# Performance work log

Hardware: AMD Instinct MI355X
Metric: run time of the kernel (lower is better)

## Reference

```python
import jax, jax.numpy as jnp
import numpy as np

H, B, S, E, V, C = 1024, 1024, 128, 6, 3, 10


def setup_inputs() -> dict:
    key = jax.random.key(0)
    ks = jax.random.split(key, 18)
    sH = 1.0 / np.sqrt(H)

    def n(k, shape, scale):
        return (jax.random.normal(k, shape, dtype=jnp.float32) * scale)

    return {
        'x': jax.random.randint(ks[0], (B, S), 0, V),
        'emb': n(ks[1], (V, E), 1.0),
        'W_gx': n(ks[2], (H, E), 1.0 / np.sqrt(E)),
        'W_gh': n(ks[3], (H, H), sH),
        'b_g': n(ks[4], (H, 1), sH),
        'W_ix': n(ks[5], (H, E), 1.0 / np.sqrt(E)),
        'W_ih': n(ks[6], (H, H), sH),
        'b_i': n(ks[7], (H, 1), sH),
        'W_fx': n(ks[8], (H, E), 1.0 / np.sqrt(E)),
        'W_fh': n(ks[9], (H, H), sH),
        'b_f': n(ks[10], (H, 1), sH),
        'W_ox': n(ks[11], (H, E), 1.0 / np.sqrt(E)),
        'W_oh': n(ks[12], (H, H), sH),
        'b_o': n(ks[13], (H, 1), sH),
        'W_ph': n(ks[14], (C, H), sH),
        'b_p': n(ks[15], (C, 1), sH),
        'h_init': n(ks[16], (H, B), 1.0),
        'c_init': n(ks[17], (H, B), 1.0),
    }


def reference(x, emb, W_gx, W_gh, b_g, W_ix, W_ih, b_i, W_fx, W_fh, b_f,
              W_ox, W_oh, b_o, W_ph, b_p, h_init, c_init):
    T = x.shape[1] - 1  # torch loop runs over seq_length - 1 steps
    e = emb[x[:, :T]]  # [B, T, E]
    # Precompute all input-to-gate projections in one batched contraction each.
    Xg = jnp.einsum('he,bte->thb', W_gx, e)  # [T, H, B]
    Xi = jnp.einsum('he,bte->thb', W_ix, e)
    Xf = jnp.einsum('he,bte->thb', W_fx, e)
    Xo = jnp.einsum('he,bte->thb', W_ox, e)

    def step(carry, xs):
        h, c = carry  # [H, B]
        xg, xi, xf, xo = xs
        g = jnp.tanh(xg + W_gh @ h + b_g)
        i = jax.nn.sigmoid(xi + W_ih @ h + b_i)
        f = jax.nn.sigmoid(xf + W_fh @ h + b_f)
        o = jax.nn.sigmoid(xo + W_oh @ h + b_o)
        c2 = g * i + c * f
        h2 = jnp.tanh(c2) * o
        return (h2, c2), None

    (h, c), _ = jax.lax.scan(step, (h_init, c_init), (Xg, Xi, Xf, Xo))
    p = W_ph @ h + b_p  # [C, B]
    return jax.nn.log_softmax(p.T, axis=-1)  # [B, C]
```

## Files before the change

### kernel.cpp

```cpp
#include <hip/hip_runtime.h>

constexpr int kH = 1024;
constexpr int kB = 1024;
constexpr int kS = 128;
constexpr int kT = 127;
constexpr int kE = 6;
constexpr int kV = 3;
constexpr int kC = 10;

typedef short s16x8 __attribute__((ext_vector_type(8)));
typedef short s16x4 __attribute__((ext_vector_type(4)));
typedef float f32x4 __attribute__((ext_vector_type(4)));
typedef int   i32x2 __attribute__((ext_vector_type(2)));
typedef int   i32x4 __attribute__((ext_vector_type(4)));
typedef unsigned short u16;

__device__ __forceinline__ float b2f(u16 u) {
    return __uint_as_float(((unsigned)u) << 16);
}
__device__ __forceinline__ u16 f2b(float f) {
    unsigned u = __float_as_uint(f);
    return (u16)((u + 0x7FFFu + ((u >> 16) & 1u)) >> 16);
}
__device__ __forceinline__ float sigmoid_fast(float x) {
    return 1.0f / (1.0f + __expf(-x));
}
__device__ __forceinline__ float tanh_fast(float x) {
    return 2.0f / (1.0f + __expf(-2.0f * x)) - 1.0f;
}
__device__ __forceinline__ float clamp30(float x) {
    return fminf(fmaxf(x, -30.0f), 30.0f);
}

__device__ __forceinline__ void async_copy16(const u16* g, u16* l) {
    __builtin_amdgcn_global_load_lds(
        (const __attribute__((address_space(1))) void*)g,
        (__attribute__((address_space(3))) void*)l, 16, 0, 0);
}

__global__ __launch_bounds__(256) void prep_weights(
    const float* __restrict__ Wgh, const float* __restrict__ Wih,
    const float* __restrict__ Wfh, const float* __restrict__ Woh,
    u16* __restrict__ wsw)
{
    unsigned grp = blockIdx.x * 256 + threadIdx.x;
    const int lane = grp & 63;
    const int lm   = lane & 15;
    const int quad = lane >> 4;
    const int k0   = (grp >> 6) & 7;
    const int g    = (grp >> 9) & 3;
    const int kc   = (grp >> 11) & 3;
    const int by   = grp >> 13;
    const float* src = (g == 0) ? Wgh : (g == 1) ? Wih : (g == 2) ? Wfh : Woh;
    const int row = by * 16 + lm;
    const int k   = kc * 256 + k0 * 32 + quad * 8;
    f32x4 v0 = *(const f32x4*)(src + (size_t)row * kH + k);
    f32x4 v1 = *(const f32x4*)(src + (size_t)row * kH + k + 4);
    s16x8 o;
#pragma unroll
    for (int j = 0; j < 4; ++j) o[j] = (short)f2b(v0[j]);
#pragma unroll
    for (int j = 0; j < 4; ++j) o[4 + j] = (short)f2b(v1[j]);
    *(s16x8*)(wsw + (size_t)grp * 8) = o;
}

__global__ __launch_bounds__(1024) void prep_hc(
    const float* __restrict__ h0, const float* __restrict__ c0,
    u16* __restrict__ hA, float* __restrict__ cT)
{
    __shared__ float th[32][33];
    __shared__ float tc[32][33];
    int b = blockIdx.x * 32 + threadIdx.x;
    int h = blockIdx.y * 32 + threadIdx.y;
    th[threadIdx.y][threadIdx.x] = h0[(size_t)h * kB + b];
    tc[threadIdx.y][threadIdx.x] = c0[(size_t)h * kB + b];
    __syncthreads();
    int ob = blockIdx.x * 32 + threadIdx.y;
    int oh = blockIdx.y * 32 + threadIdx.x;
    hA[(size_t)ob * kH + oh] = f2b(th[threadIdx.x][threadIdx.y]);
    cT[(size_t)ob * kH + oh] = tc[threadIdx.x][threadIdx.y];
}

__global__ __launch_bounds__(256) void prep_q(
    const float* __restrict__ Wgx, const float* __restrict__ Wix,
    const float* __restrict__ Wfx, const float* __restrict__ Wox,
    const float* __restrict__ bg,  const float* __restrict__ bi,
    const float* __restrict__ bf_, const float* __restrict__ bo,
    const float* __restrict__ emb, float* __restrict__ Qp,
    int* __restrict__ ctrl)
{
    int tid = blockIdx.x * blockDim.x + threadIdx.x;
    if (tid < 512) ctrl[tid] = 0;
    if (tid >= 4096) return;
    int g   = tid >> 10;
    int hr4 = (tid & 1023) >> 2;
    int v   = tid & 3;
    const float* Wx = (g == 0) ? Wgx : (g == 1) ? Wix : (g == 2) ? Wfx : Wox;
    const float* bb = (g == 0) ? bg  : (g == 1) ? bi  : (g == 2) ? bf_ : bo;
    f32x4 o;
#pragma unroll
    for (int reg = 0; reg < 4; ++reg) {
        int row = hr4 * 4 + reg;
        float s = bb[row];
        if (v < kV) {
#pragma unroll
            for (int e = 0; e < kE; ++e) s += Wx[row * kE + e] * emb[v * kE + e];
        }
        o[reg] = s;
    }
    *(f32x4*)(Qp + (size_t)tid * 4) = o;
}

__global__ __launch_bounds__(512, 2) void lstm_persist(
    const u16* __restrict__ wsw, const float* __restrict__ Qp,
    const int* __restrict__ x,
    short* __restrict__ hA, short* __restrict__ hB,
    const float* __restrict__ cT, int* __restrict__ ctrl,
    u16* __restrict__ xcb)
{
    __shared__ u16 wlds[65536];
    __shared__ int sh_ids[2];

    const int tid  = threadIdx.x;
    const int lane = tid & 63;
    const int wave = tid >> 6;
    const int lm   = lane & 15;
    const int quad = lane >> 4;

    if (tid == 0) {
        unsigned xccr;
        asm volatile("s_getreg_b32 %0, hwreg(HW_REG_XCC_ID)" : "=s"(xccr));
        int rank = atomicAdd(ctrl + 264 + (xccr & 7), 1);
        sh_ids[0] = (int)(xccr & 7);
        sh_ids[1] = rank;
    }
    __syncthreads();
    const int xcc   = sh_ids[0];
    const int rank  = sh_ids[1];
    const int p     = xcc >> 1;
    const int side  = xcc & 1;
    const int q     = side * 32 + rank;
    const int qprt  = (1 - side) * 32 + rank;
    const int r0 = q * 16;
    const int cl0 = wave * 32;
    const int c0 = p * 256 + cl0;

    int* pflag = ctrl;
    int* lcnt  = ctrl + 256;

    const u16* wswblk = wsw + (size_t)q * 65536;

#pragma unroll
    for (int rr = 0; rr < 16; ++rr) {
        const int ub = wave * 8192 + rr * 512;
        async_copy16(wswblk + ub + lane * 8, &wlds[ub]);
    }

    f32x4 creg[2];
#pragma unroll
    for (int nt = 0; nt < 2; ++nt)
        creg[nt] = *(const f32x4*)(cT +
            (size_t)(c0 + nt * 16 + lm) * kH + r0 + quad * 4);

    const int* xp0 = x + (size_t)(c0 + lm) * kS;
    const int* xp1 = x + (size_t)(c0 + 16 + lm) * kS;
    const int koff = quad * 8;

    asm volatile("s_waitcnt vmcnt(0)" ::: "memory");
    __syncthreads();

#pragma unroll 1
    for (int t = 0; t < kT; ++t) {
        short* hout = (t & 1) ? hA : hB;
        u16* xw = xcb + (size_t)(xcc * 2 + ((t + 1) & 1)) * 262144;

        if (t >= 1) {
            if (tid == 0) {
                const int* cp = lcnt + xcc;
                const int tgt = 64 * t;
                for (;;) {
                    int v;
                    asm volatile("global_load_dword %0, %1, off sc0 sc1\n\t"
                                 "s_waitcnt vmcnt(0)"
                                 : "=v"(v) : "v"(cp) : "memory");
                    if (v >= tgt) break;
                    __builtin_amdgcn_s_sleep(1);
                }
            }
            __syncthreads();
            asm volatile("buffer_inv" ::: "memory");
        }

        const u16* xr = xcb + (size_t)(xcc * 2 + (t & 1)) * 262144;
        const u16* hrow0;
        const u16* hrow1;
        if (t == 0) {
            hrow0 = (const u16*)hA + (size_t)(c0 + lm) * kH + koff;
            hrow1 = (const u16*)hA + (size_t)(c0 + 16 + lm) * kH + koff;
        } else {
            hrow0 = xr + (size_t)(cl0 + lm) * kH + koff;
            hrow1 = xr + (size_t)(cl0 + 16 + lm) * kH + koff;
        }

        s16x8 br[8][2];
#pragma unroll
        for (int s = 0; s < 6; ++s) {
            br[s][0] = *(const s16x8*)(hrow0 + s * 32);
            br[s][1] = *(const s16x8*)(hrow1 + s * 32);
        }

        int vv[2];
        {
            int v0 = xp0[t]; vv[0] = (v0 < 0) ? 0 : (v0 > kV - 1) ? (kV - 1) : v0;
            int v1 = xp1[t]; vv[1] = (v1 < 0) ? 0 : (v1 > kV - 1) ? (kV - 1) : v1;
        }
        f32x4 qv[2][4];
#pragma unroll
        for (int nt = 0; nt < 2; ++nt)
#pragma unroll
            for (int g = 0; g < 4; ++g)
                qv[nt][g] = *(const f32x4*)(Qp +
                    (size_t)(((g * 256 + q * 4 + quad) * 4 + vv[nt]) * 4));

        f32x4 acc[4][2];
        const f32x4 zero = {0.f, 0.f, 0.f, 0.f};
#pragma unroll
        for (int g = 0; g < 4; ++g)
#pragma unroll
            for (int n = 0; n < 2; ++n) acc[g][n] = zero;

#pragma unroll
        for (int k0 = 0; k0 < 32; ++k0) {
            if (k0 + 6 < 32) {
                const int s = (k0 + 6) & 7;
                br[s][0] = *(const s16x8*)(hrow0 + (k0 + 6) * 32);
                br[s][1] = *(const s16x8*)(hrow1 + (k0 + 6) * 32);
            }
            const int cur = k0 & 7;
            const int cb = (k0 >> 3) * 16384;
#pragma unroll
            for (int g = 0; g < 4; ++g) {
                const int f = cb + ((g * 8 + (k0 & 7)) * 64 + lane) * 8;
                s16x8 a = *(const s16x8*)&wlds[f];
                acc[g][0] = __builtin_amdgcn_mfma_f32_16x16x32_bf16(a, br[cur][0], acc[g][0], 0, 0, 0);
                acc[g][1] = __builtin_amdgcn_mfma_f32_16x16x32_bf16(a, br[cur][1], acc[g][1], 0, 0, 0);
            }
        }

#pragma unroll
        for (int nt = 0; nt < 2; ++nt) {
            const int cl = cl0 + nt * 16 + lm;
            const int c  = p * 256 + cl;
            const int rb = r0 + quad * 4;
            f32x4 cnew;
            s16x4 hnew;
#pragma unroll
            for (int reg = 0; reg < 4; ++reg) {
                float pg = clamp30(acc[0][nt][reg] + qv[nt][0][reg]);
                float pi = clamp30(acc[1][nt][reg] + qv[nt][1][reg]);
                float pf = clamp30(acc[2][nt][reg] + qv[nt][2][reg]);
                float po = clamp30(acc[3][nt][reg] + qv[nt][3][reg]);
                float gg = tanh_fast(pg);
                float ii = sigmoid_fast(pi);
                float ff = sigmoid_fast(pf);
                float oo = sigmoid_fast(po);
                float c2 = gg * ii + creg[nt][reg] * ff;
                c2 = fminf(fmaxf(c2, -200.0f), 200.0f);
                cnew[reg] = c2;
                hnew[reg] = (short)f2b(tanh_fast(c2) * oo);
            }
            creg[nt] = cnew;
            i32x2 hv;
            __builtin_memcpy(&hv, &hnew, 8);
            short* hp = hout + (size_t)c * kH + rb;
            asm volatile("global_store_dwordx2 %0, %1, off sc0 sc1"
                         :: "v"(hp), "v"(hv) : "memory");
            *(s16x4*)(xw + (size_t)cl * kH + rb) = hnew;
        }

        if (t < kT - 1) {
            asm volatile("s_waitcnt vmcnt(0)" ::: "memory");
            __syncthreads();
            if (tid == 0) {
                int* fp = pflag + p * 64 + q;
                int fv = t + 1;
                asm volatile("global_store_dword %0, %1, off sc0 sc1\n\t"
                             "s_waitcnt vmcnt(0)"
                             :: "v"(fp), "v"(fv) : "memory");
                atomicAdd(lcnt + xcc, 1);
                const int* pp = pflag + p * 64 + qprt;
                for (;;) {
                    int v;
                    asm volatile("global_load_dword %0, %1, off sc0 sc1\n\t"
                                 "s_waitcnt vmcnt(0)"
                                 : "=v"(v) : "v"(pp) : "memory");
                    if (v >= t + 1) break;
                    __builtin_amdgcn_s_sleep(1);
                }
            }
            __syncthreads();
            {
                const int cl   = tid >> 1;
                const int half = tid & 1;
                const short* src = hout + (size_t)(p * 256 + cl) * kH +
                                   qprt * 16 + half * 8;
                u16* dst = xw + (size_t)cl * kH + qprt * 16 + half * 8;
                i32x4 v;
                asm volatile("global_load_dwordx4 %0, %1, off sc0 sc1\n\t"
                             "s_waitcnt vmcnt(0)"
                             : "=v"(v) : "v"(src) : "memory");
                *(i32x4*)dst = v;
            }
            asm volatile("s_waitcnt vmcnt(0)" ::: "memory");
            __syncthreads();
            if (tid == 0) atomicAdd(lcnt + xcc, 1);
        }
    }
}

__global__ __launch_bounds__(256) void logits_kernel(
    const u16* __restrict__ hT, const float* __restrict__ Wph,
    const float* __restrict__ bp, float* __restrict__ out)
{
    const int wave = threadIdx.x >> 6;
    const int lane = threadIdx.x & 63;
    const int b = blockIdx.x * 4 + wave;

    const u16* hp = hT + (size_t)b * kH + lane * 16;
    float hf[16];
#pragma unroll
    for (int j = 0; j < 16; ++j) hf[j] = b2f(hp[j]);

    float p[kC];
#pragma unroll
    for (int cls = 0; cls < kC; ++cls) {
        const float* wp = Wph + (size_t)cls * kH + lane * 16;
        float s = 0.f;
#pragma unroll
        for (int j = 0; j < 16; ++j) s += hf[j] * wp[j];
#pragma unroll
        for (int off = 1; off < 64; off <<= 1) s += __shfl_xor(s, off, 64);
        p[cls] = fminf(fmaxf(s + bp[cls], -1.0e4f), 1.0e4f);
    }

    float m = p[0];
#pragma unroll
    for (int cls = 1; cls < kC; ++cls) m = fmaxf(m, p[cls]);
    float se = 0.f;
#pragma unroll
    for (int cls = 0; cls < kC; ++cls) se += __expf(p[cls] - m);
    float l = m + __logf(se);

    if (lane < kC) {
        float myp = p[0];
#pragma unroll
        for (int cls = 1; cls < kC; ++cls)
            if (lane == cls) myp = p[cls];
        out[(size_t)b * kC + lane] = myp - l;
    }
}

extern "C" void kernel_launch(void* const* d_in, const int* in_sizes, int n_in,
                              void* d_out, int out_size, void* d_ws, size_t ws_size,
                              hipStream_t stream)
{
    const int*   x   = (const int*)  d_in[0];
    const float* emb = (const float*)d_in[1];
    const float* Wgx = (const float*)d_in[2];
    const float* Wgh = (const float*)d_in[3];
    const float* bg  = (const float*)d_in[4];
    const float* Wix = (const float*)d_in[5];
    const float* Wih = (const float*)d_in[6];
    const float* bi  = (const float*)d_in[7];
    const float* Wfx = (const float*)d_in[8];
    const float* Wfh = (const float*)d_in[9];
    const float* bf_ = (const float*)d_in[10];
    const float* Wox = (const float*)d_in[11];
    const float* Woh = (const float*)d_in[12];
    const float* bo  = (const float*)d_in[13];
    const float* Wph = (const float*)d_in[14];
    const float* bp  = (const float*)d_in[15];
    const float* h0  = (const float*)d_in[16];
    const float* c0  = (const float*)d_in[17];

    char* ws = (char*)d_ws;
    float* Qp  = (float*)ws;
    u16*   hA  = (u16*)(ws + (64 << 10));
    u16*   hB  = hA + (size_t)kB * kH;
    float* cT  = (float*)(hB + (size_t)kB * kH);
    u16*   wsw = (u16*)(cT + (size_t)kB * kH);
    u16*   xcb = wsw + (size_t)64 * 65536;
    int*   ctrl = (int*)(xcb + (size_t)16 * 262144);

    prep_weights<<<dim3(2048), dim3(256), 0, stream>>>(Wgh, Wih, Wfh, Woh, wsw);
    prep_hc<<<dim3(kB / 32, kH / 32), dim3(32, 32), 0, stream>>>(h0, c0, hA, cT);
    prep_q<<<dim3(16), dim3(256), 0, stream>>>(Wgx, Wix, Wfx, Wox, bg, bi, bf_, bo,
                                               emb, Qp, ctrl);

    lstm_persist<<<dim3(256), dim3(512), 0, stream>>>(
        wsw, Qp, x, (short*)hA, (short*)hB, cT, ctrl, xcb);

    logits_kernel<<<dim3(kB / 4), dim3(256), 0, stream>>>(hB, Wph, bp, (float*)d_out);
}
```

Baseline: 3.074 ms.

## Split recurrent matmul into local and remote K halves to overlap partner exchange

The per-step h·W contraction is split into two K halves. The half whose h comes from the local XCD runs first, while the half from the partner XCD is fetched mid-step after waiting on the partner's flag. This moves the cross-XCD exchange wait out of the end-of-step critical path so it overlaps with MFMA work. The global h buffer changes to a blocked [q][b][16] layout so each exchange read is contiguous, initial h is written straight into the per-XCD exchange buffers, and a second counter is added for the extra barrier. This adds an extra intra-XCD barrier per step and more complicated flag and counter bookkeeping.

New measurement: 3.006 ms. -2.2%, faster.

```diff
diff --git a/kernel.cpp b/kernel.cpp
--- a/kernel.cpp
+++ b/kernel.cpp
@@ -66,7 +66,7 @@
 
 __global__ __launch_bounds__(1024) void prep_hc(
     const float* __restrict__ h0, const float* __restrict__ c0,
-    u16* __restrict__ hA, float* __restrict__ cT)
+    u16* __restrict__ xcb, float* __restrict__ cT)
 {
     __shared__ float th[32][33];
     __shared__ float tc[32][33];
@@ -77,8 +77,12 @@
     __syncthreads();
     int ob = blockIdx.x * 32 + threadIdx.y;
     int oh = blockIdx.y * 32 + threadIdx.x;
-    hA[(size_t)ob * kH + oh] = f2b(th[threadIdx.x][threadIdx.y]);
     cT[(size_t)ob * kH + oh] = tc[threadIdx.x][threadIdx.y];
+    u16 hv = f2b(th[threadIdx.x][threadIdx.y]);
+    int pg = ob >> 8;
+    size_t off = (size_t)(ob & 255) * kH + oh;
+    xcb[((size_t)(2 * pg) * 2 + 0) * 262144 + off] = hv;
+    xcb[((size_t)(2 * pg + 1) * 2 + 0) * 262144 + off] = hv;
 }
 
 __global__ __launch_bounds__(256) void prep_q(
@@ -111,10 +115,39 @@
     *(f32x4*)(Qp + (size_t)tid * 4) = o;
 }
 
+#define K_HALF(KB, HR0, HR1)                                                 \
+  {                                                                          \
+    s16x8 br[8][2];                                                          \
+    _Pragma("unroll")                                                        \
+    for (int s = 0; s < 6; ++s) {                                            \
+      br[s][0] = *(const s16x8*)((HR0) + s * 32);                            \
+      br[s][1] = *(const s16x8*)((HR1) + s * 32);                            \
+    }                                                                        \
+    _Pragma("unroll")                                                        \
+    for (int i = 0; i < 16; ++i) {                                           \
+      if (i + 6 < 16) {                                                      \
+        const int s = (i + 6) & 7;                                           \
+        br[s][0] = *(const s16x8*)((HR0) + (i + 6) * 32);                    \
+        br[s][1] = *(const s16x8*)((HR1) + (i + 6) * 32);                    \
+      }                                                                      \
+      const int cur = i & 7;                                                 \
+      const int cbo = (((KB) >> 3) + (i >> 3)) * 16384;                      \
+      _Pragma("unroll")                                                      \
+      for (int g = 0; g < 4; ++g) {                                          \
+        const int fo = cbo + ((g * 8 + (i & 7)) * 64 + lane) * 8;            \
+        s16x8 a = *(const s16x8*)&wlds[fo];                                  \
+        acc[g][0] = __builtin_amdgcn_mfma_f32_16x16x32_bf16(a, br[cur][0],   \
+                                                            acc[g][0], 0, 0, 0); \
+        acc[g][1] = __builtin_amdgcn_mfma_f32_16x16x32_bf16(a, br[cur][1],   \
+                                                            acc[g][1], 0, 0, 0); \
+      }                                                                      \
+    }                                                                        \
+  }
+
 __global__ __launch_bounds__(512, 2) void lstm_persist(
     const u16* __restrict__ wsw, const float* __restrict__ Qp,
     const int* __restrict__ x,
-    short* __restrict__ hA, short* __restrict__ hB,
+    u16* __restrict__ hA, u16* __restrict__ hB,
     const float* __restrict__ cT, int* __restrict__ ctrl,
     u16* __restrict__ xcb)
 {
@@ -130,7 +163,7 @@
     if (tid == 0) {
         unsigned xccr;
         asm volatile("s_getreg_b32 %0, hwreg(HW_REG_XCC_ID)" : "=s"(xccr));
-        int rank = atomicAdd(ctrl + 264 + (xccr & 7), 1);
+        int rank = atomicAdd(ctrl + 288 + (xccr & 7), 1);
         sh_ids[0] = (int)(xccr & 7);
         sh_ids[1] = rank;
     }
@@ -141,12 +174,13 @@
     const int side  = xcc & 1;
     const int q     = side * 32 + rank;
     const int qprt  = (1 - side) * 32 + rank;
-    const int r0 = q * 16;
+    const int r0  = q * 16;
     const int cl0 = wave * 32;
-    const int c0 = p * 256 + cl0;
+    const int c0  = p * 256 + cl0;
 
     int* pflag = ctrl;
     int* lcnt  = ctrl + 256;
+    int* rcnt  = ctrl + 272;
 
     const u16* wswblk = wsw + (size_t)q * 65536;
 
@@ -165,19 +199,23 @@
     const int* xp0 = x + (size_t)(c0 + lm) * kS;
     const int* xp1 = x + (size_t)(c0 + 16 + lm) * kS;
     const int koff = quad * 8;
+    const int lkb = side * 16;
+    const int rkb = (1 - side) * 16;
 
     asm volatile("s_waitcnt vmcnt(0)" ::: "memory");
     __syncthreads();
 
 #pragma unroll 1
     for (int t = 0; t < kT; ++t) {
-        short* hout = (t & 1) ? hA : hB;
-        u16* xw = xcb + (size_t)(xcc * 2 + ((t + 1) & 1)) * 262144;
+        u16* xbase = xcb + (size_t)(xcc * 2 + (t & 1)) * 262144;
+        u16* xw    = xcb + (size_t)(xcc * 2 + ((t + 1) & 1)) * 262144;
+        const u16* hsrc = (t & 1) ? hB : hA;
+        u16*       hdst = (t & 1) ? hA : hB;
 
         if (t >= 1) {
             if (tid == 0) {
                 const int* cp = lcnt + xcc;
-                const int tgt = 64 * t;
+                const int tgt = 32 * t;
                 for (;;) {
                     int v;
                     asm volatile("global_load_dword %0, %1, off sc0 sc1\n\t"
@@ -191,24 +229,6 @@
             asm volatile("buffer_inv" ::: "memory");
         }
 
-        const u16* xr = xcb + (size_t)(xcc * 2 + (t & 1)) * 262144;
-        const u16* hrow0;
-        const u16* hrow1;
-        if (t == 0) {
-            hrow0 = (const u16*)hA + (size_t)(c0 + lm) * kH + koff;
-            hrow1 = (const u16*)hA + (size_t)(c0 + 16 + lm) * kH + koff;
-        } else {
-            hrow0 = xr + (size_t)(cl0 + lm) * kH + koff;
-            hrow1 = xr + (size_t)(cl0 + 16 + lm) * kH + koff;
-        }
-
-        s16x8 br[8][2];
-#pragma unroll
-        for (int s = 0; s < 6; ++s) {
-            br[s][0] = *(const s16x8*)(hrow0 + s * 32);
-            br[s][1] = *(const s16x8*)(hrow1 + s * 32);
-        }
-
         int vv[2];
         {
             int v0 = xp0[t]; vv[0] = (v0 < 0) ? 0 : (v0 > kV - 1) ? (kV - 1) : v0;
@@ -229,22 +249,60 @@
 #pragma unroll
             for (int n = 0; n < 2; ++n) acc[g][n] = zero;
 
-#pragma unroll
-        for (int k0 = 0; k0 < 32; ++k0) {
-            if (k0 + 6 < 32) {
-                const int s = (k0 + 6) & 7;
-                br[s][0] = *(const s16x8*)(hrow0 + (k0 + 6) * 32);
-                br[s][1] = *(const s16x8*)(hrow1 + (k0 + 6) * 32);
-            }
-            const int cur = k0 & 7;
-            const int cb = (k0 >> 3) * 16384;
-#pragma unroll
-            for (int g = 0; g < 4; ++g) {
-                const int f = cb + ((g * 8 + (k0 & 7)) * 64 + lane) * 8;
-                s16x8 a = *(const s16x8*)&wlds[f];
-                acc[g][0] = __builtin_amdgcn_mfma_f32_16x16x32_bf16(a, br[cur][0], acc[g][0], 0, 0, 0);
-                acc[g][1] = __builtin_amdgcn_mfma_f32_16x16x32_bf16(a, br[cur][1], acc[g][1], 0, 0, 0);
-            }
+        {
+            const u16* hr0 = xbase + (size_t)(cl0 + lm) * kH + lkb * 32 + koff;
+            const u16* hr1 = xbase + (size_t)(cl0 + 16 + lm) * kH + lkb * 32 + koff;
+            K_HALF(lkb, hr0, hr1)
+        }
+
+        if (t >= 1) {
+            if (tid == 0) {
+                const int* pp = pflag + p * 64 + qprt;
+                for (;;) {
+                    int v;
+                    asm volatile("global_load_dword %0, %1, off sc0 sc1\n\t"
+                                 "s_waitcnt vmcnt(0)"
+                                 : "=v"(v) : "v"(pp) : "memory");
+                    if (v >= t) break;
+                    __builtin_amdgcn_s_sleep(1);
+                }
+            }
+            __syncthreads();
+            {
+                const int cl = tid >> 1;
+                const int hf = tid & 1;
+                const u16* srcp = hsrc +
+                    ((size_t)qprt * 1024 + p * 256 + cl) * 16 + hf * 8;
+                u16* dstp = xbase + (size_t)cl * kH + qprt * 16 + hf * 8;
+                i32x4 v;
+                asm volatile("global_load_dwordx4 %0, %1, off sc0 sc1\n\t"
+                             "s_waitcnt vmcnt(0)"
+                             : "=&v"(v) : "v"(srcp) : "memory");
+                *(i32x4*)dstp = v;
+            }
+            asm volatile("s_waitcnt vmcnt(0)" ::: "memory");
+            __syncthreads();
+            if (tid == 0) {
+                atomicAdd(rcnt + xcc, 1);
+                const int* cp = rcnt + xcc;
+                const int tgt = 32 * t;
+                for (;;) {
+                    int v;
+                    asm volatile("global_load_dword %0, %1, off sc0 sc1\n\t"
+                                 "s_waitcnt vmcnt(0)"
+                                 : "=v"(v) : "v"(cp) : "memory");
+                    if (v >= tgt) break;
+                    __builtin_amdgcn_s_sleep(1);
+                }
+            }
+            __syncthreads();
+            asm volatile("buffer_inv" ::: "memory");
+        }
+
+        {
+            const u16* hr0 = xbase + (size_t)(cl0 + lm) * kH + rkb * 32 + koff;
+            const u16* hr1 = xbase + (size_t)(cl0 + 16 + lm) * kH + rkb * 32 + koff;
+            K_HALF(rkb, hr0, hr1)
         }
 
 #pragma unroll
@@ -272,7 +330,7 @@
             creg[nt] = cnew;
             i32x2 hv;
             __builtin_memcpy(&hv, &hnew, 8);
-            short* hp = hout + (size_t)c * kH + rb;
+            short* hp = (short*)hdst + ((size_t)q * 1024 + c) * 16 + quad * 4;
             asm volatile("global_store_dwordx2 %0, %1, off sc0 sc1"
                          :: "v"(hp), "v"(hv) : "memory");
             *(s16x4*)(xw + (size_t)cl * kH + rb) = hnew;
@@ -288,32 +346,7 @@
                              "s_waitcnt vmcnt(0)"
                              :: "v"(fp), "v"(fv) : "memory");
                 atomicAdd(lcnt + xcc, 1);
-                const int* pp = pflag + p * 64 + qprt;
-                for (;;) {
-                    int v;
-                    asm volatile("global_load_dword %0, %1, off sc0 sc1\n\t"
-                                 "s_waitcnt vmcnt(0)"
-                                 : "=v"(v) : "v"(pp) : "memory");
-                    if (v >= t + 1) break;
-                    __builtin_amdgcn_s_sleep(1);
-                }
-            }
-            __syncthreads();
-            {
-                const int cl   = tid >> 1;
-                const int half = tid & 1;
-                const short* src = hout + (size_t)(p * 256 + cl) * kH +
-                                   qprt * 16 + half * 8;
-                u16* dst = xw + (size_t)cl * kH + qprt * 16 + half * 8;
-                i32x4 v;
-                asm volatile("global_load_dwordx4 %0, %1, off sc0 sc1\n\t"
-                             "s_waitcnt vmcnt(0)"
-                             : "=v"(v) : "v"(src) : "memory");
-                *(i32x4*)dst = v;
-            }
-            asm volatile("s_waitcnt vmcnt(0)" ::: "memory");
-            __syncthreads();
-            if (tid == 0) atomicAdd(lcnt + xcc, 1);
+            }
         }
     }
 }
@@ -326,7 +359,7 @@
     const int lane = threadIdx.x & 63;
     const int b = blockIdx.x * 4 + wave;
 
-    const u16* hp = hT + (size_t)b * kH + lane * 16;
+    const u16* hp = hT + ((size_t)lane * 1024 + b) * 16;
     float hf[16];
 #pragma unroll
     for (int j = 0; j < 16; ++j) hf[j] = b2f(hp[j]);
@@ -393,12 +426,12 @@
     int*   ctrl = (int*)(xcb + (size_t)16 * 262144);
 
     prep_weights<<<dim3(2048), dim3(256), 0, stream>>>(Wgh, Wih, Wfh, Woh, wsw);
-    prep_hc<<<dim3(kB / 32, kH / 32), dim3(32, 32), 0, stream>>>(h0, c0, hA, cT);
+    prep_hc<<<dim3(kB / 32, kH / 32), dim3(32, 32), 0, stream>>>(h0, c0, xcb, cT);
     prep_q<<<dim3(16), dim3(256), 0, stream>>>(Wgx, Wix, Wfx, Wox, bg, bi, bf_, bo,
                                                emb, Qp, ctrl);
 
     lstm_persist<<<dim3(256), dim3(512), 0, stream>>>(
-        wsw, Qp, x, (short*)hA, (short*)hB, cT, ctrl, xcb);
+        wsw, Qp, x, hA, hB, cT, ctrl, xcb);
 
     logits_kernel<<<dim3(kB / 4), dim3(256), 0, stream>>>(hB, Wph, bp, (float*)d_out);
 }
```
